# Performance work log

Measured on AMD Instinct MI355X. Metric: run time of the kernel, lower is better.

## Reference

```python
import jax, jax.numpy as jnp
import numpy as np

N = 2_000_000   # total nodes across the batch of graphs
D = 128         # node feature dim (in_features in PSRNet)
G = 256         # number of graphs in the batch (graph.batch.max()+1)


def setup_inputs() -> dict:
    key = jax.random.key(0)
    k1, k2, k3, k4 = jax.random.split(key, 4)
    x = jax.random.normal(k1, (N, D), dtype=jnp.float32)
    batch = jnp.sort(jax.random.randint(k2, (N,), 0, G)).astype(jnp.int64)
    # top_net = Linear(128,64) -> ReLU -> Dropout(eval: identity) -> Linear(64,1)
    W1 = jax.random.normal(k3, (D, D // 2), dtype=jnp.float32) * 0.05
    b1 = jnp.zeros((D // 2,), dtype=jnp.float32)
    W2 = jax.random.normal(k4, (D // 2, 1), dtype=jnp.float32) * 0.05
    b2 = jnp.zeros((1,), dtype=jnp.float32)
    return {"x": x, "batch": batch, "W1": W1, "b1": b1, "W2": W2, "b2": b2}


def reference(x, batch, W1, b1, W2, b2):
    # scatter-add sum and count per graph, then mean (matches torch scatter_add_ + div)
    sums = jax.ops.segment_sum(x, batch, num_segments=G)                       # [G, D]
    counts = jax.ops.segment_sum(jnp.ones((x.shape[0],), x.dtype), batch,
                                 num_segments=G)                               # [G]
    mean = sums / counts[:, None]                                              # [G, D]
    # top_net MLP head (dropout is identity in eval)
    h = jax.nn.relu(mean @ W1 + b1)                                            # [G, D//2]
    return h @ W2 + b2                                                         # [G, 1]
```

## Files before the change

### kernel.cpp

```cpp
#include <hip/hip_runtime.h>

#define G_NUM 256
#define D_DIM 128

__global__ void zero_ws_kernel(float* __restrict__ ws, int n) {
    int i = blockIdx.x * blockDim.x + threadIdx.x;
    if (i < n) ws[i] = 0.0f;
}

__global__ __launch_bounds__(256) void seg_sum_kernel(
    const float4* __restrict__ x4, const int* __restrict__ batch,
    float* __restrict__ sums, unsigned int* __restrict__ counts,
    int n_rows, int rows_per_block)
{
    const int lane = threadIdx.x & 31;
    const int sub  = threadIdx.x >> 5;
    const int row_start = blockIdx.x * rows_per_block;
    const int row_end   = min(n_rows, row_start + rows_per_block);

    int g_cur = -1;
    float4 acc = make_float4(0.f, 0.f, 0.f, 0.f);
    unsigned int cnt = 0;

    for (int r = row_start + sub; r < row_end; r += 8) {
        const int b = batch[r];
        if (b != g_cur) {
            if (g_cur >= 0) {
                float* dst = sums + (size_t)g_cur * D_DIM + lane * 4;
                atomicAdd(dst + 0, acc.x);
                atomicAdd(dst + 1, acc.y);
                atomicAdd(dst + 2, acc.z);
                atomicAdd(dst + 3, acc.w);
                if (lane == 0) atomicAdd(&counts[g_cur], cnt);
            }
            g_cur = b;
            acc = make_float4(0.f, 0.f, 0.f, 0.f);
            cnt = 0;
        }
        const float4 v = x4[(size_t)r * (D_DIM / 4) + lane];
        acc.x += v.x; acc.y += v.y; acc.z += v.z; acc.w += v.w;
        ++cnt;
    }
    if (g_cur >= 0) {
        float* dst = sums + (size_t)g_cur * D_DIM + lane * 4;
        atomicAdd(dst + 0, acc.x);
        atomicAdd(dst + 1, acc.y);
        atomicAdd(dst + 2, acc.z);
        atomicAdd(dst + 3, acc.w);
        if (lane == 0) atomicAdd(&counts[g_cur], cnt);
    }
}

__global__ __launch_bounds__(64) void mlp_kernel(
    const float* __restrict__ sums, const unsigned int* __restrict__ counts,
    const float* __restrict__ W1, const float* __restrict__ b1,
    const float* __restrict__ W2, const float* __restrict__ b2,
    float* __restrict__ out)
{
    const int g = blockIdx.x;
    const int j = threadIdx.x;
    __shared__ float mean_s[D_DIM];

    const float c = (float)counts[g];
    mean_s[j]      = sums[(size_t)g * D_DIM + j]      / c;
    mean_s[j + 64] = sums[(size_t)g * D_DIM + j + 64] / c;
    __syncthreads();

    float acc = b1[j];
#pragma unroll 8
    for (int k = 0; k < D_DIM; ++k)
        acc += mean_s[k] * W1[k * (D_DIM / 2) + j];

    float p = fmaxf(acc, 0.0f) * W2[j];

    for (int off = 32; off > 0; off >>= 1)
        p += __shfl_down(p, off, 64);

    if (j == 0) out[g] = p + b2[0];
}

extern "C" void kernel_launch(void* const* d_in, const int* in_sizes, int n_in,
                              void* d_out, int out_size, void* d_ws, size_t ws_size,
                              hipStream_t stream) {
    const float* x     = (const float*)d_in[0];
    const int*   batch = (const int*)d_in[1];
    const float* W1    = (const float*)d_in[2];
    const float* b1    = (const float*)d_in[3];
    const float* W2    = (const float*)d_in[4];
    const float* b2    = (const float*)d_in[5];
    float*       out   = (float*)d_out;

    const int n_rows = in_sizes[1];

    float*        sums   = (float*)d_ws;
    unsigned int* counts = (unsigned int*)((char*)d_ws + (size_t)G_NUM * D_DIM * sizeof(float));

    const int zero_n = G_NUM * D_DIM + G_NUM;
    zero_ws_kernel<<<(zero_n + 255) / 256, 256, 0, stream>>>((float*)d_ws, zero_n);

    const int nblocks = 2048;
    const int rows_per_block = (n_rows + nblocks - 1) / nblocks;
    seg_sum_kernel<<<nblocks, 256, 0, stream>>>(
        (const float4*)x, batch, sums, counts, n_rows, rows_per_block);

    mlp_kernel<<<G_NUM, 64, 0, stream>>>(sums, counts, W1, b1, W2, b2, out);
}
```

Baseline: 1.314 ms.

## Find segment boundaries by binary search and unroll row accumulation by four

```diff
diff --git a/kernel.cpp b/kernel.cpp
--- a/kernel.cpp
+++ b/kernel.cpp
@@ -17,37 +17,50 @@
     const int sub  = threadIdx.x >> 5;
     const int row_start = blockIdx.x * rows_per_block;
     const int row_end   = min(n_rows, row_start + rows_per_block);
+    if (row_start >= row_end) return;
 
-    int g_cur = -1;
-    float4 acc = make_float4(0.f, 0.f, 0.f, 0.f);
-    unsigned int cnt = 0;
+    const int b_last = batch[row_end - 1];
 
-    for (int r = row_start + sub; r < row_end; r += 8) {
-        const int b = batch[r];
-        if (b != g_cur) {
-            if (g_cur >= 0) {
-                float* dst = sums + (size_t)g_cur * D_DIM + lane * 4;
-                atomicAdd(dst + 0, acc.x);
-                atomicAdd(dst + 1, acc.y);
-                atomicAdd(dst + 2, acc.z);
-                atomicAdd(dst + 3, acc.w);
-                if (lane == 0) atomicAdd(&counts[g_cur], cnt);
+    int rs = row_start;
+    while (rs < row_end) {
+        const int b = batch[rs];
+        int re;
+        if (b == b_last) {
+            re = row_end;
+        } else {
+            int lo = rs + 1, hi = row_end - 1;
+            while (lo < hi) {
+                const int mid = (lo + hi) >> 1;
+                if (batch[mid] == b) lo = mid + 1; else hi = mid;
             }
-            g_cur = b;
-            acc = make_float4(0.f, 0.f, 0.f, 0.f);
-            cnt = 0;
+            re = lo;
         }
-        const float4 v = x4[(size_t)r * (D_DIM / 4) + lane];
-        acc.x += v.x; acc.y += v.y; acc.z += v.z; acc.w += v.w;
-        ++cnt;
-    }
-    if (g_cur >= 0) {
-        float* dst = sums + (size_t)g_cur * D_DIM + lane * 4;
+
+        float4 acc = make_float4(0.f, 0.f, 0.f, 0.f);
+        int r = rs + sub;
+        for (; r + 24 < re; r += 32) {
+            const float4 v0 = x4[(size_t)(r     ) * (D_DIM / 4) + lane];
+            const float4 v1 = x4[(size_t)(r +  8) * (D_DIM / 4) + lane];
+            const float4 v2 = x4[(size_t)(r + 16) * (D_DIM / 4) + lane];
+            const float4 v3 = x4[(size_t)(r + 24) * (D_DIM / 4) + lane];
+            acc.x += (v0.x + v1.x) + (v2.x + v3.x);
+            acc.y += (v0.y + v1.y) + (v2.y + v3.y);
+            acc.z += (v0.z + v1.z) + (v2.z + v3.z);
+            acc.w += (v0.w + v1.w) + (v2.w + v3.w);
+        }
+        for (; r < re; r += 8) {
+            const float4 v = x4[(size_t)r * (D_DIM / 4) + lane];
+            acc.x += v.x; acc.y += v.y; acc.z += v.z; acc.w += v.w;
+        }
+
+        float* dst = sums + (size_t)b * D_DIM + lane * 4;
         atomicAdd(dst + 0, acc.x);
         atomicAdd(dst + 1, acc.y);
         atomicAdd(dst + 2, acc.z);
         atomicAdd(dst + 3, acc.w);
-        if (lane == 0) atomicAdd(&counts[g_cur], cnt);
+        if (threadIdx.x == 0) atomicAdd(&counts[b], (unsigned int)(re - rs));
+
+        rs = re;
     }
 }
 
```

New measurement: 1.286 ms. 1.02x faster.
